# Kernel tuning notes

Hardware: AMD Instinct MI355X
Metric: run time of the kernel (lower is better)

Reference implementation:

```python
import jax, jax.numpy as jnp
import numpy as np

LATENT = 128
K_SUBTREES = 64      # children of the root '&&'
DEPTH = 11           # perfect binary subtree depth -> 2**11 = 2048 leaves each
N_NODES = 50000      # program-graph node embedding rows
N_TOKENS = 32        # len(LIST_PREDICATES) + len(LIST_OP)


def setup_inputs() -> dict:
    key = jax.random.key(0)
    ks = jax.random.split(key, 16)
    L = LATENT
    s = 0.08  # keep tanh/sigmoid out of saturation, like trained weights
    return {
        "node_embedding": jax.random.normal(ks[0], (N_NODES, L), jnp.float32) * 0.5,
        "init_embedding": jax.random.normal(ks[1], (1, L), jnp.float32) * 0.5,
        "char_embedding": jax.random.normal(ks[2], (N_TOKENS, L), jnp.float32) * 0.5,
        # stacked gate weights, y = x @ W + b
        # W_child order: ilh, irh, lflh, lfrh, rflh, rfrh, ulh, urh
        "W_child": jax.random.normal(ks[3], (8, L, L), jnp.float32) * s,
        "b_child": jax.random.normal(ks[4], (8, L), jnp.float32) * s,
        # W_x order: ix, fx, ux
        "W_x": jax.random.normal(ks[5], (3, L, L), jnp.float32) * s,
        "b_x": jax.random.normal(ks[6], (3, L), jnp.float32) * s,
        # W_leaf order: cx, ox
        "W_leaf": jax.random.normal(ks[7], (2, L, L), jnp.float32) * s,
        "b_leaf": jax.random.normal(ks[8], (2, L), jnp.float32) * s,
        # W_and order: and_transform_c, and_transform_h
        "W_and": jax.random.normal(ks[9], (2, L, L), jnp.float32) * s,
        "b_and": jax.random.normal(ks[10], (2, L), jnp.float32) * s,
        "W_oend": jax.random.normal(ks[11], (3 * L, L), jnp.float32) * s,
        "b_oend": jax.random.normal(ks[12], (L,), jnp.float32) * s,
        "leaf_idx": jax.random.randint(ks[13], (K_SUBTREES, 2 ** DEPTH), 0, N_NODES, jnp.int32),
        "op_idx": jax.random.randint(ks[14], (K_SUBTREES, 2 ** DEPTH - 1), 0, N_TOKENS, jnp.int32),
    }


def reference(node_embedding, init_embedding, char_embedding,
              W_child, b_child, W_x, b_x, W_leaf, b_leaf,
              W_and, b_and, W_oend, b_oend, leaf_idx, op_idx):
    n_leaves = leaf_idx.shape[1]
    depth = int(np.log2(n_leaves))

    # --- leaves: c = cx(x); h = sigmoid(ox(x)) * tanh(c) ---
    x = node_embedding[leaf_idx]                      # [K, M, L]
    c = x @ W_leaf[0] + b_leaf[0]
    h = jax.nn.sigmoid(x @ W_leaf[1] + b_leaf[1]) * jnp.tanh(c)

    # --- internal binary Tree-LSTM cells, level by level (bottom-up) ---
    start = 0
    for d in range(depth):
        m = n_leaves >> (d + 1)                       # nodes at this level
        xe = char_embedding[op_idx[:, start:start + m]]  # [K, m, L]
        start += m
        lc, rc = c[:, 0::2], c[:, 1::2]
        lh, rh = h[:, 0::2], h[:, 1::2]
        # fused gate projections: [3|4, K, m, L]
        gx = jnp.einsum('kml,gld->gkmd', xe, W_x) + b_x[:, None, None, :]
        gl = jnp.einsum('kml,gld->gkmd', lh, W_child[0::2]) + b_child[0::2, None, None, :]
        gr = jnp.einsum('kml,gld->gkmd', rh, W_child[1::2]) + b_child[1::2, None, None, :]
        i = jax.nn.sigmoid(gx[0] + gl[0] + gr[0])          # ix + ilh + irh
        lf = jax.nn.sigmoid(gx[1] + gl[1] + gr[1])         # fx + lflh + lfrh
        rf = jax.nn.sigmoid(gx[1] + gl[2] + gr[2])         # fx + rflh + rfrh
        u = jnp.tanh(gx[2] + gl[3] + gr[3])                # ux + ulh + urh
        c = i * u + lf * lc + rf * rc
        h = jnp.tanh(c)

    # --- root '&&': transform, min-pool over children, output gate ---
    c2 = c[:, 0] @ W_and[0] + b_and[0]                 # [K, L]
    h2 = h[:, 0] @ W_and[1] + b_and[1]
    cmin = jnp.min(c2, axis=0, keepdims=True)          # [1, L]
    hmin = jnp.min(h2, axis=0, keepdims=True)
    s = jnp.concatenate([init_embedding, cmin, hmin], axis=1)  # [1, 3L]
    return jnp.tanh(s @ W_oend + b_oend)
```

## Files before the change

kernel.cpp:

```cpp
#include <hip/hip_runtime.h>

#define NNODES 50000

typedef _Float16 half8 __attribute__((ext_vector_type(8)));
typedef float f32x4 __attribute__((ext_vector_type(4)));

__device__ __forceinline__ float sigm(float x)   { return 1.f / (1.f + __expf(-x)); }
__device__ __forceinline__ float tanh_f(float x) { float e = __expf(2.f * x); return 1.f - 2.f / (e + 1.f); }

__global__ __launch_bounds__(256) void k_prep(const float* __restrict__ Wc,
                                              const float* __restrict__ Wl,
                                              const float* __restrict__ ce,
                                              const float* __restrict__ Wx,
                                              const float* __restrict__ bx,
                                              const float* __restrict__ bc,
                                              _Float16* __restrict__ WpT,
                                              _Float16* __restrict__ WlT) {
    int b = blockIdx.x;
    if (b < 512) {
        int i = b * 256 + threadIdx.x;
        int c = i >> 8, k = i & 255;
        int g = c >> 7, d = c & 127;
        float v = (k < 128) ? Wc[(2 * g) * 16384 + k * 128 + d]
                            : Wc[(2 * g + 1) * 16384 + (k - 128) * 128 + d];
        WpT[c * 288 + k] = (_Float16)v;
    } else if (b < 640) {
        int i = (b - 512) * 256 + threadIdx.x;
        int c = i >> 7, k = i & 127;
        WlT[i] = (_Float16)Wl[(c >> 7) * 16384 + k * 128 + (c & 127)];
    } else {
        int i = (b - 640) * 256 + threadIdx.x;
        int tt = i >> 9, c = i & 511;
        int g = c >> 7, d = c & 127;
        int gx = (g == 0) ? 0 : ((g == 3) ? 2 : 1);
        float acc = bx[gx * 128 + d] + bc[(2 * g) * 128 + d] + bc[(2 * g + 1) * 128 + d];
        const float* x = ce + tt * 128;
        const float* w = Wx + gx * 16384 + d;
        for (int l = 0; l < 128; ++l) acc += x[l] * w[l * 128];
        WpT[c * 288 + 256 + tt] = (_Float16)acc;
    }
}

__global__ __launch_bounds__(256) void k_prep_nodes(const float* __restrict__ ne,
                                                    const _Float16* __restrict__ WlT,
                                                    const float* __restrict__ bl,
                                                    _Float16* __restrict__ c_tab,
                                                    _Float16* __restrict__ h_tab) {
    const int t = threadIdx.x;
    const int w = t >> 6, l = t & 63;
    const int lr = l & 15, lq = l >> 4;
    const int nb = blockIdx.x * 32;

    int arow[2];
#pragma unroll
    for (int rt = 0; rt < 2; ++rt) {
        int r = nb + rt * 16 + lr;
        arow[rt] = (r < NNODES) ? r : (NNODES - 1);
    }

    f32x4 acc[2][2][2];
#pragma unroll
    for (int rt = 0; rt < 2; ++rt)
#pragma unroll
        for (int g = 0; g < 2; ++g)
#pragma unroll
            for (int ti = 0; ti < 2; ++ti) acc[rt][g][ti] = (f32x4)0.f;

#pragma unroll
    for (int kk = 0; kk < 4; ++kk) {
        half8 af[2];
#pragma unroll
        for (int rt = 0; rt < 2; ++rt) {
            const float* src = ne + (size_t)arow[rt] * 128 + kk * 32 + lq * 8;
            float4 f0 = *(const float4*)src;
            float4 f1 = *(const float4*)(src + 4);
            half8 v;
            v[0] = (_Float16)f0.x; v[1] = (_Float16)f0.y; v[2] = (_Float16)f0.z; v[3] = (_Float16)f0.w;
            v[4] = (_Float16)f1.x; v[5] = (_Float16)f1.y; v[6] = (_Float16)f1.z; v[7] = (_Float16)f1.w;
            af[rt] = v;
        }
#pragma unroll
        for (int g = 0; g < 2; ++g)
#pragma unroll
            for (int ti = 0; ti < 2; ++ti) {
                int col = g * 128 + w * 32 + ti * 16 + lr;
                half8 bb = *(const half8*)(WlT + col * 128 + kk * 32 + lq * 8);
#pragma unroll
                for (int rt = 0; rt < 2; ++rt)
                    acc[rt][g][ti] = __builtin_amdgcn_mfma_f32_16x16x32_f16(af[rt], bb, acc[rt][g][ti], 0, 0, 0);
            }
    }

#pragma unroll
    for (int rt = 0; rt < 2; ++rt)
#pragma unroll
        for (int j = 0; j < 4; ++j) {
            int r = nb + rt * 16 + lq * 4 + j;
            if (r < NNODES) {
#pragma unroll
                for (int ti = 0; ti < 2; ++ti) {
                    int d = w * 32 + ti * 16 + lr;
                    float cc = acc[rt][0][ti][j] + bl[d];
                    float hp = acc[rt][1][ti][j] + bl[128 + d];
                    c_tab[(size_t)r * 128 + d] = (_Float16)cc;
                    h_tab[(size_t)r * 128 + d] = (_Float16)(sigm(hp) * tanh_f(cc));
                }
            }
        }
}


struct LoQ { half8 af[8]; _Float16 lcv[4], rcv[4]; };

__device__ __forceinline__ void lo_gather(int qb,
                                          const _Float16* __restrict__ c_tab,
                                          const _Float16* __restrict__ h_tab,
                                          const int* s_leaf,
                                          int lq, int lr, int dcol, LoQ& s) {
#pragma unroll
    for (int j = 0; j < 4; ++j) {
        int p = qb + lq * 4 + j;
        s.lcv[j] = c_tab[(size_t)s_leaf[2 * p] * 128 + dcol];
        s.rcv[j] = c_tab[(size_t)s_leaf[2 * p + 1] * 128 + dcol];
    }
    const int pg = qb + lr;
    const int gl = s_leaf[2 * pg], gr = s_leaf[2 * pg + 1];
#pragma unroll
    for (int kk = 0; kk < 8; ++kk) {
        int row = (kk < 4) ? gl : gr;
        s.af[kk] = *(const half8*)(h_tab + (size_t)row * 128 + (kk & 3) * 32 + lq * 8);
    }
}

__device__ __forceinline__ void lo_mfma(const LoQ& s, int qb, const _Float16* s_oh,
                                        const half8 (&B)[9][4], int lq, int lr,
                                        f32x4 (&acc)[4]) {
#pragma unroll
    for (int g = 0; g < 4; ++g) acc[g] = (f32x4)0.f;
#pragma unroll
    for (int kk = 0; kk < 9; ++kk) {
        half8 a = (kk < 8) ? s.af[kk]
                           : *(const half8*)(s_oh + (qb + lr) * 36 + lq * 8);
#pragma unroll
        for (int g = 0; g < 4; ++g)
            acc[g] = __builtin_amdgcn_mfma_f32_16x16x32_f16(a, B[kk][g], acc[g], 0, 0, 0);
    }
}

__device__ __forceinline__ void lo_epi(const f32x4 (&acc)[4], const LoQ& s, int qb,
                                       _Float16* hA, _Float16* cA, int lq, int dcol) {
#pragma unroll
    for (int j = 0; j < 4; ++j) {
        int p = qb + lq * 4 + j;
        float cc = sigm(acc[0][j]) * tanh_f(acc[3][j])
                 + sigm(acc[1][j]) * (float)s.lcv[j]
                 + sigm(acc[2][j]) * (float)s.rcv[j];
        cA[p * 132 + dcol] = (_Float16)cc;
        hA[p * 128 + (dcol ^ ((p & 15) << 3))] = (_Float16)tanh_f(cc);
    }
}

__device__ __forceinline__ void lds_pass2(int opoff,
                                          const _Float16* hS, const _Float16* cS,
                                          _Float16* hD, _Float16* cD,
                                          const _Float16* s_oh,
                                          const half8 (&B)[9][4],
                                          int lq, int lr, int dcol) {
    f32x4 acc[2][4];
#pragma unroll
    for (int rt = 0; rt < 2; ++rt)
#pragma unroll
        for (int g = 0; g < 4; ++g) acc[rt][g] = (f32x4)0.f;

#pragma unroll
    for (int kk = 0; kk < 9; ++kk) {
        half8 a[2];
        if (kk < 8) {
            int side = kk >> 2, ko = (kk & 3) * 32 + lq * 8;
#pragma unroll
            for (int rt = 0; rt < 2; ++rt) {
                int child = 2 * (rt * 16 + lr) + side;
                a[rt] = *(const half8*)(hS + child * 128 + (ko ^ ((child & 15) << 3)));
            }
        } else {
            a[0] = *(const half8*)(s_oh + (opoff + lr) * 36 + lq * 8);
            a[1] = *(const half8*)(s_oh + (opoff + 16 + lr) * 36 + lq * 8);
        }
#pragma unroll
        for (int rt = 0; rt < 2; ++rt)
#pragma unroll
            for (int g = 0; g < 4; ++g)
                acc[rt][g] = __builtin_amdgcn_mfma_f32_16x16x32_f16(a[rt], B[kk][g], acc[rt][g], 0, 0, 0);
    }

#pragma unroll
    for (int rt = 0; rt < 2; ++rt)
#pragma unroll
        for (int j = 0; j < 4; ++j) {
            int p = rt * 16 + lq * 4 + j;
            float vi = acc[rt][0][j], vl = acc[rt][1][j];
            float vr = acc[rt][2][j], vu = acc[rt][3][j];
            float lc = (float)cS[(2 * p) * 132 + dcol];
            float rc = (float)cS[(2 * p + 1) * 132 + dcol];
            float cc = sigm(vi) * tanh_f(vu) + sigm(vl) * lc + sigm(vr) * rc;
            cD[p * 132 + dcol] = (_Float16)cc;
            hD[p * 128 + (dcol ^ ((p & 15) << 3))] = (_Float16)tanh_f(cc);
        }
}

template <int NP, bool G3OUT>
__device__ __forceinline__ void lds_pass(int opoff,
                                         const _Float16* hS, const _Float16* cS,
                                         _Float16* hD, _Float16* cD,
                                         float* __restrict__ gc, _Float16* __restrict__ gh,
                                         int growbase,
                                         const _Float16* s_oh, const half8 (&B)[9][4],
                                         int lq, int lr, int dcol) {
    const int pidx = (NP >= 16) ? lr : (lr & (NP - 1));
    f32x4 acc[4];
#pragma unroll
    for (int g = 0; g < 4; ++g) acc[g] = (f32x4)0.f;
#pragma unroll
    for (int kk = 0; kk < 9; ++kk) {
        half8 a;
        if (kk < 8) {
            int side = kk >> 2, ko = (kk & 3) * 32 + lq * 8;
            int child = 2 * pidx + side;
            a = *(const half8*)(hS + child * 128 + (ko ^ ((child & 15) << 3)));
        } else {
            a = *(const half8*)(s_oh + (opoff + pidx) * 36 + lq * 8);
        }
#pragma unroll
        for (int g = 0; g < 4; ++g)
            acc[g] = __builtin_amdgcn_mfma_f32_16x16x32_f16(a, B[kk][g], acc[g], 0, 0, 0);
    }
#pragma unroll
    for (int j = 0; j < 4; ++j) {
        int p = lq * 4 + j;
        if (p < NP) {
            float vi = acc[0][j], vl = acc[1][j], vr = acc[2][j], vu = acc[3][j];
            float lc = (float)cS[(2 * p) * 132 + dcol];
            float rc = (float)cS[(2 * p + 1) * 132 + dcol];
            float cc = sigm(vi) * tanh_f(vu) + sigm(vl) * lc + sigm(vr) * rc;
            if constexpr (G3OUT) {
                gc[(size_t)(growbase + p) * 128 + dcol] = cc;
                gh[(size_t)(growbase + p) * 128 + dcol] = (_Float16)tanh_f(cc);
            } else {
                cD[p * 132 + dcol] = (_Float16)cc;
                hD[p * 128 + (dcol ^ ((p & 15) << 3))] = (_Float16)tanh_f(cc);
            }
        }
    }
}

__global__ __launch_bounds__(512, 2) void k_lo(const _Float16* __restrict__ c_tab,
                                               const _Float16* __restrict__ h_tab,
                                               const int* __restrict__ leaf_idx,
                                               const int* __restrict__ op_idx,
                                               const _Float16* __restrict__ WpT,
                                               float* __restrict__ g3c,
                                               _Float16* __restrict__ g3h) {
    __shared__ int s_leaf[128];
    __shared__ int s_op[120];
    __shared__ _Float16 s_oh[120 * 36];
    __shared__ _Float16 hA[64 * 128], cA[64 * 132];
    __shared__ _Float16 hB[32 * 128], cB[32 * 132];

    const int t = threadIdx.x;
    const int w = t >> 6, l = t & 63, lr = l & 15, lq = l >> 4;
    const int ks = blockIdx.x >> 4, seg = blockIdx.x & 15;
    const int dcol = w * 16 + lr;

    if (t < 128) s_leaf[t] = leaf_idx[ks * 2048 + seg * 128 + t];
    else if (t < 192) s_op[t - 128] = op_idx[ks * 2047 + seg * 64 + (t - 128)];
    else if (t < 224) s_op[64 + t - 192] = op_idx[ks * 2047 + 1024 + seg * 32 + (t - 192)];
    else if (t < 240) s_op[96 + t - 224] = op_idx[ks * 2047 + 1536 + seg * 16 + (t - 224)];
    else if (t < 248) s_op[112 + t - 240] = op_idx[ks * 2047 + 1792 + seg * 8 + (t - 240)];

    half8 B[9][4];
#pragma unroll
    for (int kk = 0; kk < 9; ++kk)
#pragma unroll
        for (int g = 0; g < 4; ++g)
            B[kk][g] = *(const half8*)(WpT + (g * 128 + dcol) * 288 + kk * 32 + lq * 8);

    __syncthreads();
    for (int i = t; i < 120 * 32; i += 512) {
        int p = i >> 5, k = i & 31;
        s_oh[p * 36 + k] = (_Float16)((k == s_op[p]) ? 1.f : 0.f);
    }
    __syncthreads();

    LoQ q0, q1;
    f32x4 acc[4];
    lo_gather(0, c_tab, h_tab, s_leaf, lq, lr, dcol, q0);

    lo_mfma(q0, 0, s_oh, B, lq, lr, acc);
    lo_gather(16, c_tab, h_tab, s_leaf, lq, lr, dcol, q1);
    lo_epi(acc, q0, 0, hA, cA, lq, dcol);

    lo_mfma(q1, 16, s_oh, B, lq, lr, acc);
    lo_gather(32, c_tab, h_tab, s_leaf, lq, lr, dcol, q0);
    lo_epi(acc, q1, 16, hA, cA, lq, dcol);

    lo_mfma(q0, 32, s_oh, B, lq, lr, acc);
    lo_gather(48, c_tab, h_tab, s_leaf, lq, lr, dcol, q1);
    lo_epi(acc, q0, 32, hA, cA, lq, dcol);

    lo_mfma(q1, 48, s_oh, B, lq, lr, acc);
    lo_epi(acc, q1, 48, hA, cA, lq, dcol);
    __syncthreads();

    lds_pass2(64, hA, cA, hB, cB, s_oh, B, lq, lr, dcol);
    __syncthreads();

    lds_pass<16, false>(96, hB, cB, hA, cA, nullptr, nullptr, 0, s_oh, B, lq, lr, dcol);
    __syncthreads();

    lds_pass<8, true>(112, hA, cA, nullptr, nullptr, g3c, g3h, blockIdx.x * 8,
                      s_oh, B, lq, lr, dcol);
}

template <int NRT, bool GSRC>
__device__ __forceinline__ void tail_pass(int np, int pass0, int opoff,
                                          const _Float16* hS, const _Float16* cS,
                                          const _Float16* __restrict__ gh,
                                          const float* __restrict__ gc, int rowbase,
                                          _Float16* hD, _Float16* cD,
                                          const _Float16* s_oh,
                                          const half8 (&B)[9][4],
                                          const int* , int w, int lq, int lr) {
    f32x4 acc[NRT][4];
#pragma unroll
    for (int rt = 0; rt < NRT; ++rt)
#pragma unroll
        for (int g = 0; g < 4; ++g) acc[rt][g] = (f32x4)0.f;

    int pidx[NRT];
#pragma unroll
    for (int rt = 0; rt < NRT; ++rt) {
        int p = pass0 + rt * 16 + lr;
        pidx[rt] = (p < np) ? p : (np - 1);
    }

#pragma unroll
    for (int kk = 0; kk < 9; ++kk) {
        half8 a[NRT];
        if (kk < 8) {
            int side = kk >> 2, ko = (kk & 3) * 32 + lq * 8;
#pragma unroll
            for (int rt = 0; rt < NRT; ++rt) {
                int child = 2 * pidx[rt] + side;
                if constexpr (GSRC)
                    a[rt] = *(const half8*)(gh + (size_t)(rowbase + child) * 128 + ko);
                else
                    a[rt] = *(const half8*)(hS + child * 128 + (ko ^ ((child & 15) << 3)));
            }
        } else {
#pragma unroll
            for (int rt = 0; rt < NRT; ++rt)
                a[rt] = *(const half8*)(s_oh + (opoff + pidx[rt]) * 36 + lq * 8);
        }
#pragma unroll
        for (int rt = 0; rt < NRT; ++rt)
#pragma unroll
            for (int g = 0; g < 4; ++g)
                acc[rt][g] = __builtin_amdgcn_mfma_f32_16x16x32_f16(a[rt], B[kk][g], acc[rt][g], 0, 0, 0);
    }

    const int d = w * 16 + lr;
#pragma unroll
    for (int rt = 0; rt < NRT; ++rt)
#pragma unroll
        for (int j = 0; j < 4; ++j) {
            int p = pass0 + rt * 16 + lq * 4 + j;
            if (p < np) {
                float vi = acc[rt][0][j], vl = acc[rt][1][j];
                float vr = acc[rt][2][j], vu = acc[rt][3][j];
                float lc, rc;
                if constexpr (GSRC) {
                    lc = gc[(size_t)(rowbase + 2 * p) * 128 + d];
                    rc = gc[(size_t)(rowbase + 2 * p + 1) * 128 + d];
                } else {
                    lc = (float)cS[(2 * p) * 132 + d];
                    rc = (float)cS[(2 * p + 1) * 132 + d];
                }
                float cc = sigm(vi) * tanh_f(vu) + sigm(vl) * lc + sigm(vr) * rc;
                cD[p * 132 + d] = (_Float16)cc;
                hD[p * 128 + (d ^ ((p & 15) << 3))] = (_Float16)tanh_f(cc);
            }
        }
}

__global__ __launch_bounds__(512, 2) void k_tail4(const float* __restrict__ g3c,
                                                  const _Float16* __restrict__ g3h,
                                                  const int* __restrict__ op_idx,
                                                  const _Float16* __restrict__ WpT,
                                                  const float* __restrict__ Wa,
                                                  const float* __restrict__ ba,
                                                  float* __restrict__ c2,
                                                  float* __restrict__ h2) {
    __shared__ int s_op[128];
    __shared__ _Float16 s_oh[127 * 36];
    __shared__ _Float16 hA[64 * 128], cA[64 * 132];
    __shared__ _Float16 hB[32 * 128], cB[32 * 132];
    const int t = threadIdx.x, w = t >> 6, l = t & 63, lr = l & 15, lq = l >> 4;
    const int tree = blockIdx.x;
    const int rb = tree * 128;

    if (t < 127) s_op[t] = op_idx[tree * 2047 + 1920 + t];

    half8 B[9][4];
#pragma unroll
    for (int kk = 0; kk < 9; ++kk)
#pragma unroll
        for (int g = 0; g < 4; ++g)
            B[kk][g] = *(const half8*)(WpT + (g * 128 + w * 16 + lr) * 288 + kk * 32 + lq * 8);

    __syncthreads();
    for (int i = t; i < 127 * 32; i += 512) {
        int p = i >> 5, k = i & 31;
        s_oh[p * 36 + k] = (_Float16)((k == s_op[p]) ? 1.f : 0.f);
    }
    __syncthreads();

    tail_pass<2, true>(64,  0, 0, nullptr, nullptr, g3h, g3c, rb, hA, cA, s_oh, B, s_op, w, lq, lr);
    tail_pass<2, true>(64, 32, 0, nullptr, nullptr, g3h, g3c, rb, hA, cA, s_oh, B, s_op, w, lq, lr);
    __syncthreads();
    tail_pass<2, false>(32, 0, 64, hA, cA, nullptr, nullptr, 0, hB, cB, s_oh, B, s_op, w, lq, lr);
    __syncthreads();
    tail_pass<1, false>(16, 0,  96, hB, cB, nullptr, nullptr, 0, hA, cA, s_oh, B, s_op, w, lq, lr);
    __syncthreads();
    tail_pass<1, false>( 8, 0, 112, hA, cA, nullptr, nullptr, 0, hB, cB, s_oh, B, s_op, w, lq, lr);
    __syncthreads();
    tail_pass<1, false>( 4, 0, 120, hB, cB, nullptr, nullptr, 0, hA, cA, s_oh, B, s_op, w, lq, lr);
    __syncthreads();
    tail_pass<1, false>( 2, 0, 124, hA, cA, nullptr, nullptr, 0, hB, cB, s_oh, B, s_op, w, lq, lr);
    __syncthreads();
    tail_pass<1, false>( 1, 0, 126, hB, cB, nullptr, nullptr, 0, hA, cA, s_oh, B, s_op, w, lq, lr);
    __syncthreads();

    if (t < 256) {
        int dd = t & 127;
        if (t < 128) {
            float a = ba[dd];
            for (int ll = 0; ll < 128; ++ll) a += (float)cA[ll] * Wa[ll * 128 + dd];
            c2[tree * 128 + dd] = a;
        } else {
            float a = ba[128 + dd];
            for (int ll = 0; ll < 128; ++ll) a += (float)hA[ll] * Wa[16384 + ll * 128 + dd];
            h2[tree * 128 + dd] = a;
        }
    }
}

__global__ __launch_bounds__(128) void k_final(const float* __restrict__ c2,
                                               const float* __restrict__ h2,
                                               const float* __restrict__ init_e,
                                               const float* __restrict__ Wo,
                                               const float* __restrict__ bo,
                                               float* __restrict__ out) {
    __shared__ float s[384];
    const int d = threadIdx.x;
    float cm = c2[d], hm = h2[d];
    for (int k = 1; k < 64; ++k) {
        cm = fminf(cm, c2[k * 128 + d]);
        hm = fminf(hm, h2[k * 128 + d]);
    }
    s[d] = init_e[d];
    s[128 + d] = cm;
    s[256 + d] = hm;
    __syncthreads();
    float a = bo[d];
    for (int l = 0; l < 384; ++l) a += s[l] * Wo[l * 128 + d];
    out[d] = tanhf(a);
}

extern "C" void kernel_launch(void* const* d_in, const int* in_sizes, int n_in,
                              void* d_out, int out_size, void* d_ws, size_t ws_size,
                              hipStream_t stream) {
    const float* node_emb = (const float*)d_in[0];
    const float* init_emb = (const float*)d_in[1];
    const float* char_emb = (const float*)d_in[2];
    const float* W_child  = (const float*)d_in[3];
    const float* b_child  = (const float*)d_in[4];
    const float* W_x      = (const float*)d_in[5];
    const float* b_x      = (const float*)d_in[6];
    const float* W_leaf   = (const float*)d_in[7];
    const float* b_leaf   = (const float*)d_in[8];
    const float* W_and    = (const float*)d_in[9];
    const float* b_and    = (const float*)d_in[10];
    const float* W_oend   = (const float*)d_in[11];
    const float* b_oend   = (const float*)d_in[12];
    const int* leaf_idx   = (const int*)d_in[13];
    const int* op_idx     = (const int*)d_in[14];
    float* out = (float*)d_out;
    (void)in_sizes; (void)n_in; (void)out_size; (void)ws_size;

    char* p = (char*)d_ws;
    auto carve = [&](size_t bytes) { char* r = p; p += (bytes + 255) & ~255ull; return r; };
    _Float16* WpT   = (_Float16*)carve((size_t)512 * 288 * 2);
    _Float16* WlT   = (_Float16*)carve((size_t)256 * 128 * 2);
    _Float16* c_tab = (_Float16*)carve((size_t)NNODES * 128 * 2);
    _Float16* h_tab = (_Float16*)carve((size_t)NNODES * 128 * 2);
    float*    g3c   = (float*)carve((size_t)8192 * 128 * 4);
    _Float16* g3h   = (_Float16*)carve((size_t)8192 * 128 * 2);
    float*    c2    = (float*)carve(64 * 128 * 4);
    float*    h2    = (float*)carve(64 * 128 * 4);

    k_prep      <<<704, 256, 0, stream>>>(W_child, W_leaf, char_emb, W_x, b_x, b_child, WpT, WlT);
    k_prep_nodes<<<(NNODES + 31) / 32, 256, 0, stream>>>(node_emb, WlT, b_leaf, c_tab, h_tab);

    k_lo   <<<1024, 512, 0, stream>>>(c_tab, h_tab, leaf_idx, op_idx, WpT, g3c, g3h);
    k_tail4<<<  64, 512, 0, stream>>>(g3c, g3h, op_idx, WpT, W_and, b_and, c2, h2);
    k_final<<<1, 128, 0, stream>>>(c2, h2, init_emb, W_oend, b_oend, out);
}
```

Baseline: 185.3 us.

## Move one more tree level from tail kernel into the leaf-level kernel

Each k_lo block now handles 256 leaves (eight blocks per subtree, 512 blocks in total) and reduces them through five levels in LDS. Level 4 is written to global memory instead of level 3. The single-block-per-tree tail kernel therefore processes 64 instead of 128 nodes per tree and runs one fewer serial pass, which shrinks the poorly parallel tail stage. In exchange, k_lo's LDS footprint roughly doubles, which likely prevents two blocks per CU despite the launch bounds and halves the number of blocks available to hide gather latency.

```diff
diff --git a/kernel.cpp b/kernel.cpp
--- a/kernel.cpp
+++ b/kernel.cpp
@@ -160,7 +160,7 @@
     }
 }
 
-__device__ __forceinline__ void lds_pass2(int opoff,
+__device__ __forceinline__ void lds_pass2(int pass0, int opoff,
                                           const _Float16* hS, const _Float16* cS,
                                           _Float16* hD, _Float16* cD,
                                           const _Float16* s_oh,
@@ -179,12 +179,12 @@
             int side = kk >> 2, ko = (kk & 3) * 32 + lq * 8;
 #pragma unroll
             for (int rt = 0; rt < 2; ++rt) {
-                int child = 2 * (rt * 16 + lr) + side;
+                int child = 2 * (pass0 + rt * 16 + lr) + side;
                 a[rt] = *(const half8*)(hS + child * 128 + (ko ^ ((child & 15) << 3)));
             }
         } else {
-            a[0] = *(const half8*)(s_oh + (opoff + lr) * 36 + lq * 8);
-            a[1] = *(const half8*)(s_oh + (opoff + 16 + lr) * 36 + lq * 8);
+            a[0] = *(const half8*)(s_oh + (opoff + pass0 + lr) * 36 + lq * 8);
+            a[1] = *(const half8*)(s_oh + (opoff + pass0 + 16 + lr) * 36 + lq * 8);
         }
 #pragma unroll
         for (int rt = 0; rt < 2; ++rt)
@@ -197,7 +197,7 @@
     for (int rt = 0; rt < 2; ++rt)
 #pragma unroll
         for (int j = 0; j < 4; ++j) {
-            int p = rt * 16 + lq * 4 + j;
+            int p = pass0 + rt * 16 + lq * 4 + j;
             float vi = acc[rt][0][j], vl = acc[rt][1][j];
             float vr = acc[rt][2][j], vu = acc[rt][3][j];
             float lc = (float)cS[(2 * p) * 132 + dcol];
@@ -258,24 +258,25 @@
                                                const int* __restrict__ leaf_idx,
                                                const int* __restrict__ op_idx,
                                                const _Float16* __restrict__ WpT,
-                                               float* __restrict__ g3c,
-                                               _Float16* __restrict__ g3h) {
-    __shared__ int s_leaf[128];
-    __shared__ int s_op[120];
-    __shared__ _Float16 s_oh[120 * 36];
-    __shared__ _Float16 hA[64 * 128], cA[64 * 132];
-    __shared__ _Float16 hB[32 * 128], cB[32 * 132];
+                                               float* __restrict__ g4c,
+                                               _Float16* __restrict__ g4h) {
+    __shared__ int s_leaf[256];
+    __shared__ int s_op[248];
+    __shared__ _Float16 s_oh[248 * 36];
+    __shared__ _Float16 hA[128 * 128], cA[128 * 132];
+    __shared__ _Float16 hB[64 * 128],  cB[64 * 132];
 
     const int t = threadIdx.x;
     const int w = t >> 6, l = t & 63, lr = l & 15, lq = l >> 4;
-    const int ks = blockIdx.x >> 4, seg = blockIdx.x & 15;
+    const int ks = blockIdx.x >> 3, oct = blockIdx.x & 7;
     const int dcol = w * 16 + lr;
 
-    if (t < 128) s_leaf[t] = leaf_idx[ks * 2048 + seg * 128 + t];
-    else if (t < 192) s_op[t - 128] = op_idx[ks * 2047 + seg * 64 + (t - 128)];
-    else if (t < 224) s_op[64 + t - 192] = op_idx[ks * 2047 + 1024 + seg * 32 + (t - 192)];
-    else if (t < 240) s_op[96 + t - 224] = op_idx[ks * 2047 + 1536 + seg * 16 + (t - 224)];
-    else if (t < 248) s_op[112 + t - 240] = op_idx[ks * 2047 + 1792 + seg * 8 + (t - 240)];
+    if (t < 256) s_leaf[t] = leaf_idx[ks * 2048 + oct * 256 + t];
+    else if (t < 384) s_op[t - 256] = op_idx[ks * 2047 + oct * 128 + (t - 256)];
+    else if (t < 448) s_op[128 + t - 384] = op_idx[ks * 2047 + 1024 + oct * 64 + (t - 384)];
+    else if (t < 480) s_op[192 + t - 448] = op_idx[ks * 2047 + 1536 + oct * 32 + (t - 448)];
+    else if (t < 496) s_op[224 + t - 480] = op_idx[ks * 2047 + 1792 + oct * 16 + (t - 480)];
+    else if (t < 504) s_op[240 + t - 496] = op_idx[ks * 2047 + 1920 + oct * 8 + (t - 496)];
 
     half8 B[9][4];
 #pragma unroll
@@ -285,7 +286,7 @@
             B[kk][g] = *(const half8*)(WpT + (g * 128 + dcol) * 288 + kk * 32 + lq * 8);
 
     __syncthreads();
-    for (int i = t; i < 120 * 32; i += 512) {
+    for (int i = t; i < 248 * 32; i += 512) {
         int p = i >> 5, k = i & 31;
         s_oh[p * 36 + k] = (_Float16)((k == s_op[p]) ? 1.f : 0.f);
     }
@@ -295,29 +296,49 @@
     f32x4 acc[4];
     lo_gather(0, c_tab, h_tab, s_leaf, lq, lr, dcol, q0);
 
-    lo_mfma(q0, 0, s_oh, B, lq, lr, acc);
+    lo_mfma(q0,   0, s_oh, B, lq, lr, acc);
     lo_gather(16, c_tab, h_tab, s_leaf, lq, lr, dcol, q1);
-    lo_epi(acc, q0, 0, hA, cA, lq, dcol);
-
-    lo_mfma(q1, 16, s_oh, B, lq, lr, acc);
+    lo_epi(acc, q0,   0, hA, cA, lq, dcol);
+
+    lo_mfma(q1,  16, s_oh, B, lq, lr, acc);
     lo_gather(32, c_tab, h_tab, s_leaf, lq, lr, dcol, q0);
-    lo_epi(acc, q1, 16, hA, cA, lq, dcol);
-
-    lo_mfma(q0, 32, s_oh, B, lq, lr, acc);
+    lo_epi(acc, q1,  16, hA, cA, lq, dcol);
+
+    lo_mfma(q0,  32, s_oh, B, lq, lr, acc);
     lo_gather(48, c_tab, h_tab, s_leaf, lq, lr, dcol, q1);
-    lo_epi(acc, q0, 32, hA, cA, lq, dcol);
-
-    lo_mfma(q1, 48, s_oh, B, lq, lr, acc);
-    lo_epi(acc, q1, 48, hA, cA, lq, dcol);
-    __syncthreads();
-
-    lds_pass2(64, hA, cA, hB, cB, s_oh, B, lq, lr, dcol);
-    __syncthreads();
-
-    lds_pass<16, false>(96, hB, cB, hA, cA, nullptr, nullptr, 0, s_oh, B, lq, lr, dcol);
-    __syncthreads();
-
-    lds_pass<8, true>(112, hA, cA, nullptr, nullptr, g3c, g3h, blockIdx.x * 8,
+    lo_epi(acc, q0,  32, hA, cA, lq, dcol);
+
+    lo_mfma(q1,  48, s_oh, B, lq, lr, acc);
+    lo_gather(64, c_tab, h_tab, s_leaf, lq, lr, dcol, q0);
+    lo_epi(acc, q1,  48, hA, cA, lq, dcol);
+
+    lo_mfma(q0,  64, s_oh, B, lq, lr, acc);
+    lo_gather(80, c_tab, h_tab, s_leaf, lq, lr, dcol, q1);
+    lo_epi(acc, q0,  64, hA, cA, lq, dcol);
+
+    lo_mfma(q1,  80, s_oh, B, lq, lr, acc);
+    lo_gather(96, c_tab, h_tab, s_leaf, lq, lr, dcol, q0);
+    lo_epi(acc, q1,  80, hA, cA, lq, dcol);
+
+    lo_mfma(q0,  96, s_oh, B, lq, lr, acc);
+    lo_gather(112, c_tab, h_tab, s_leaf, lq, lr, dcol, q1);
+    lo_epi(acc, q0,  96, hA, cA, lq, dcol);
+
+    lo_mfma(q1, 112, s_oh, B, lq, lr, acc);
+    lo_epi(acc, q1, 112, hA, cA, lq, dcol);
+    __syncthreads();
+
+    lds_pass2( 0, 128, hA, cA, hB, cB, s_oh, B, lq, lr, dcol);
+    lds_pass2(32, 128, hA, cA, hB, cB, s_oh, B, lq, lr, dcol);
+    __syncthreads();
+
+    lds_pass2(0, 192, hB, cB, hA, cA, s_oh, B, lq, lr, dcol);
+    __syncthreads();
+
+    lds_pass<16, false>(224, hA, cA, hB, cB, nullptr, nullptr, 0, s_oh, B, lq, lr, dcol);
+    __syncthreads();
+
+    lds_pass<8, true>(240, hB, cB, nullptr, nullptr, g4c, g4h, blockIdx.x * 8,
                       s_oh, B, lq, lr, dcol);
 }
 
@@ -329,7 +350,7 @@
                                           _Float16* hD, _Float16* cD,
                                           const _Float16* s_oh,
                                           const half8 (&B)[9][4],
-                                          const int* , int w, int lq, int lr) {
+                                          int w, int lq, int lr) {
     f32x4 acc[NRT][4];
 #pragma unroll
     for (int rt = 0; rt < NRT; ++rt)
@@ -392,23 +413,23 @@
         }
 }
 
-__global__ __launch_bounds__(512, 2) void k_tail4(const float* __restrict__ g3c,
-                                                  const _Float16* __restrict__ g3h,
+__global__ __launch_bounds__(512, 2) void k_tail5(const float* __restrict__ g4c,
+                                                  const _Float16* __restrict__ g4h,
                                                   const int* __restrict__ op_idx,
                                                   const _Float16* __restrict__ WpT,
                                                   const float* __restrict__ Wa,
                                                   const float* __restrict__ ba,
                                                   float* __restrict__ c2,
                                                   float* __restrict__ h2) {
-    __shared__ int s_op[128];
-    __shared__ _Float16 s_oh[127 * 36];
-    __shared__ _Float16 hA[64 * 128], cA[64 * 132];
-    __shared__ _Float16 hB[32 * 128], cB[32 * 132];
+    __shared__ int s_op[64];
+    __shared__ _Float16 s_oh[63 * 36];
+    __shared__ _Float16 hA[32 * 128], cA[32 * 132];
+    __shared__ _Float16 hB[16 * 128], cB[16 * 132];
     const int t = threadIdx.x, w = t >> 6, l = t & 63, lr = l & 15, lq = l >> 4;
     const int tree = blockIdx.x;
-    const int rb = tree * 128;
-
-    if (t < 127) s_op[t] = op_idx[tree * 2047 + 1920 + t];
+    const int rb = tree * 64;
+
+    if (t < 63) s_op[t] = op_idx[tree * 2047 + 1984 + t];
 
     half8 B[9][4];
 #pragma unroll
@@ -418,37 +439,34 @@
             B[kk][g] = *(const half8*)(WpT + (g * 128 + w * 16 + lr) * 288 + kk * 32 + lq * 8);
 
     __syncthreads();
-    for (int i = t; i < 127 * 32; i += 512) {
+    for (int i = t; i < 63 * 32; i += 512) {
         int p = i >> 5, k = i & 31;
         s_oh[p * 36 + k] = (_Float16)((k == s_op[p]) ? 1.f : 0.f);
     }
     __syncthreads();
 
-    tail_pass<2, true>(64,  0, 0, nullptr, nullptr, g3h, g3c, rb, hA, cA, s_oh, B, s_op, w, lq, lr);
-    tail_pass<2, true>(64, 32, 0, nullptr, nullptr, g3h, g3c, rb, hA, cA, s_oh, B, s_op, w, lq, lr);
-    __syncthreads();
-    tail_pass<2, false>(32, 0, 64, hA, cA, nullptr, nullptr, 0, hB, cB, s_oh, B, s_op, w, lq, lr);
-    __syncthreads();
-    tail_pass<1, false>(16, 0,  96, hB, cB, nullptr, nullptr, 0, hA, cA, s_oh, B, s_op, w, lq, lr);
-    __syncthreads();
-    tail_pass<1, false>( 8, 0, 112, hA, cA, nullptr, nullptr, 0, hB, cB, s_oh, B, s_op, w, lq, lr);
-    __syncthreads();
-    tail_pass<1, false>( 4, 0, 120, hB, cB, nullptr, nullptr, 0, hA, cA, s_oh, B, s_op, w, lq, lr);
-    __syncthreads();
-    tail_pass<1, false>( 2, 0, 124, hA, cA, nullptr, nullptr, 0, hB, cB, s_oh, B, s_op, w, lq, lr);
-    __syncthreads();
-    tail_pass<1, false>( 1, 0, 126, hB, cB, nullptr, nullptr, 0, hA, cA, s_oh, B, s_op, w, lq, lr);
+    tail_pass<2, true>(32, 0, 0, nullptr, nullptr, g4h, g4c, rb, hA, cA, s_oh, B, w, lq, lr);
+    __syncthreads();
+    tail_pass<1, false>(16, 0, 32, hA, cA, nullptr, nullptr, 0, hB, cB, s_oh, B, w, lq, lr);
+    __syncthreads();
+    tail_pass<1, false>( 8, 0, 48, hB, cB, nullptr, nullptr, 0, hA, cA, s_oh, B, w, lq, lr);
+    __syncthreads();
+    tail_pass<1, false>( 4, 0, 56, hA, cA, nullptr, nullptr, 0, hB, cB, s_oh, B, w, lq, lr);
+    __syncthreads();
+    tail_pass<1, false>( 2, 0, 60, hB, cB, nullptr, nullptr, 0, hA, cA, s_oh, B, w, lq, lr);
+    __syncthreads();
+    tail_pass<1, false>( 1, 0, 62, hA, cA, nullptr, nullptr, 0, hB, cB, s_oh, B, w, lq, lr);
     __syncthreads();
 
     if (t < 256) {
         int dd = t & 127;
         if (t < 128) {
             float a = ba[dd];
-            for (int ll = 0; ll < 128; ++ll) a += (float)cA[ll] * Wa[ll * 128 + dd];
+            for (int ll = 0; ll < 128; ++ll) a += (float)cB[ll] * Wa[ll * 128 + dd];
             c2[tree * 128 + dd] = a;
         } else {
             float a = ba[128 + dd];
-            for (int ll = 0; ll < 128; ++ll) a += (float)hA[ll] * Wa[16384 + ll * 128 + dd];
+            for (int ll = 0; ll < 128; ++ll) a += (float)hB[ll] * Wa[16384 + ll * 128 + dd];
             h2[tree * 128 + dd] = a;
         }
     }
@@ -503,15 +521,15 @@
     _Float16* WlT   = (_Float16*)carve((size_t)256 * 128 * 2);
     _Float16* c_tab = (_Float16*)carve((size_t)NNODES * 128 * 2);
     _Float16* h_tab = (_Float16*)carve((size_t)NNODES * 128 * 2);
-    float*    g3c   = (float*)carve((size_t)8192 * 128 * 4);
-    _Float16* g3h   = (_Float16*)carve((size_t)8192 * 128 * 2);
+    float*    g4c   = (float*)carve((size_t)4096 * 128 * 4);
+    _Float16* g4h   = (_Float16*)carve((size_t)4096 * 128 * 2);
     float*    c2    = (float*)carve(64 * 128 * 4);
     float*    h2    = (float*)carve(64 * 128 * 4);
 
     k_prep      <<<704, 256, 0, stream>>>(W_child, W_leaf, char_emb, W_x, b_x, b_child, WpT, WlT);
     k_prep_nodes<<<(NNODES + 31) / 32, 256, 0, stream>>>(node_emb, WlT, b_leaf, c_tab, h_tab);
 
-    k_lo   <<<1024, 512, 0, stream>>>(c_tab, h_tab, leaf_idx, op_idx, WpT, g3c, g3h);
-    k_tail4<<<  64, 512, 0, stream>>>(g3c, g3h, op_idx, WpT, W_and, b_and, c2, h2);
+    k_lo   <<<512, 512, 0, stream>>>(c_tab, h_tab, leaf_idx, op_idx, WpT, g4c, g4h);
+    k_tail5<<< 64, 512, 0, stream>>>(g4c, g4h, op_idx, WpT, W_and, b_and, c2, h2);
     k_final<<<1, 128, 0, stream>>>(c2, h2, init_emb, W_oend, b_oend, out);
 }
```

New measurement: 175.5 us. -5.3%, faster.
